# Kernel optimization log

Measured on AMD Instinct MI355X. Metric: run time of the kernel, lower is better.

## Reference

```python
import jax, jax.numpy as jnp
import numpy as np
from jax import lax

B, L = 2, 2048          # batch, seq_len
V = 256                 # vocab
DM = 256                # d_model
DI = 512                # d_inner = 2*d_model (expand=2)
N = 16                  # d_state
R = 16                  # dt_rank = ceil(d_model/16)
K = 4                   # d_conv
NL = 4                  # n_layer
DO = 10                 # d_output
EPS = 1e-5


def setup_inputs() -> dict:
    key = jax.random.key(0)
    ks = jax.random.split(key, 12)
    f = lambda k, shp, s=0.02: (jax.random.normal(k, shp, jnp.float32) * s)
    A_init = jnp.log(jnp.tile(jnp.arange(1, N + 1, dtype=jnp.float32)[None, None, :], (NL, DI, 1)))
    return {
        "input_ids": jax.random.randint(ks[0], (B, L), 0, V, dtype=jnp.int32),
        "emb": f(ks[1], (V, DM)),
        "norm_w": jnp.ones((NL, DM), jnp.float32),
        "norm_b": jnp.zeros((NL, DM), jnp.float32),
        "in_proj_w": f(ks[2], (NL, 2 * DI, DM)),
        "conv_w": f(ks[3], (NL, DI, K), 0.1),
        "conv_b": jnp.zeros((NL, DI), jnp.float32),
        "x_proj_w": f(ks[4], (NL, R + 2 * N, DI)),
        "dt_proj_w": f(ks[5], (NL, DI, R), 0.1),
        "dt_proj_b": f(ks[6], (NL, DI), 0.1),
        "A_log": A_init,
        "Dp": jnp.ones((NL, DI), jnp.float32),
        "out_proj_w": f(ks[7], (NL, DM, DI)),
        "normf_w": jnp.ones((DM,), jnp.float32),
        "normf_b": jnp.zeros((DM,), jnp.float32),
        "dec_w": f(ks[8], (DO, DM)),
        "dec_b": jnp.zeros((DO,), jnp.float32),
    }


def _layer_norm(x, w, b):
    m = x.mean(-1, keepdims=True)
    v = jnp.mean((x - m) ** 2, axis=-1, keepdims=True)
    return (x - m) * lax.rsqrt(v + EPS) * w + b


def _causal_dwconv(x, w, b):
    # x: [B,L,DI], w: [DI,K] depthwise causal conv
    xt = x.transpose(0, 2, 1)  # [B,DI,L]
    out = lax.conv_general_dilated(xt, w[:, None, :], (1,), [(K - 1, 0)],
                                   feature_group_count=DI)
    return (out + b[None, :, None]).transpose(0, 2, 1)


def _selective_scan(deltaA, deltaBu, C):
    # deltaA, deltaBu: [B,L,DI,N]; C: [B,L,N]
    def step(h, inp):
        dA, dBu, c = inp
        h = dA * h + dBu                       # [B,DI,N]
        y = jnp.einsum('bdn,bn->bd', h, c)
        return h, y
    h0 = jnp.zeros(deltaA.shape[:1] + deltaA.shape[2:], deltaA.dtype)
    _, ys = lax.scan(step, h0, (deltaA.transpose(1, 0, 2, 3),
                                deltaBu.transpose(1, 0, 2, 3),
                                C.transpose(1, 0, 2)))
    return ys.transpose(1, 0, 2)  # [B,L,DI]


def _mixer(x, in_w, cw, cb, xp_w, dt_w, dt_b, A_log, Dp, out_w):
    xz = jnp.einsum('bld,ed->ble', x, in_w)        # [B,L,2*DI]
    xm, z = jnp.split(xz, 2, axis=-1)
    xc = jax.nn.silu(_causal_dwconv(xm, cw, cb))   # [B,L,DI]
    x_dbl = jnp.einsum('bld,ed->ble', xc, xp_w)    # [B,L,R+2N]
    dt, Bm, Cm = jnp.split(x_dbl, [R, R + N], axis=-1)
    delta = jax.nn.softplus(jnp.einsum('blr,dr->bld', dt, dt_w) + dt_b)  # [B,L,DI]
    A = -jnp.exp(A_log)                            # [DI,N]
    deltaA = jnp.exp(delta[..., None] * A)         # [B,L,DI,N]
    deltaBu = delta[..., None] * Bm[:, :, None, :] * xc[..., None]
    y = _selective_scan(deltaA, deltaBu, Cm)       # [B,L,DI]
    y = y + Dp * xc
    y = y * jax.nn.silu(z)
    return jnp.einsum('bld,ed->ble', y, out_w)     # [B,L,DM]


def reference(input_ids, emb, norm_w, norm_b, in_proj_w, conv_w, conv_b,
              x_proj_w, dt_proj_w, dt_proj_b, A_log, Dp, out_proj_w,
              normf_w, normf_b, dec_w, dec_b):
    hidden = emb[input_ids]                        # [B,L,DM]
    residual = None
    for i in range(NL):
        residual = hidden + residual if residual is not None else hidden
        h = _layer_norm(residual, norm_w[i], norm_b[i])
        hidden = _mixer(h, in_proj_w[i], conv_w[i], conv_b[i], x_proj_w[i],
                        dt_proj_w[i], dt_proj_b[i], A_log[i], Dp[i], out_proj_w[i])
    residual = hidden + residual
    hidden = _layer_norm(residual, normf_w, normf_b)
    pooled = hidden.mean(axis=1)                   # [B,DM]
    return pooled @ dec_w.T + dec_b                # [B,DO]
```

## Files before the change

### kernel.cpp

```cpp
#include <hip/hip_runtime.h>
#include <hip/hip_bf16.h>

#define BB 2
#define LL 2048
#define DM 256
#define DI 512
#define NST 16
#define RDT 16
#define KC 4
#define NLAY 4
#define DOUT 10
#define XDIM 48
#define TOK (BB*LL)
#define EPSF 1e-5f
#define CHUNK 16
#define NCH (LL/CHUNK)

typedef __bf16 bf16x8 __attribute__((ext_vector_type(8)));
typedef __bf16 bf16x4 __attribute__((ext_vector_type(4)));
typedef float  f32x4  __attribute__((ext_vector_type(4)));

__device__ __forceinline__ float sigmoid_f(float x) { return 1.0f / (1.0f + __expf(-x)); }

__global__ void cast_w_kernel(const float* __restrict__ a, const float* __restrict__ b,
                              const float* __restrict__ c,
                              __bf16* __restrict__ ab, __bf16* __restrict__ bb,
                              __bf16* __restrict__ cbf,
                              int na, int nb, int nc) {
  int stride = gridDim.x * 256;
  for (int i = blockIdx.x*256 + threadIdx.x; i < na; i += stride) ab[i] = (__bf16)a[i];
  for (int i = blockIdx.x*256 + threadIdx.x; i < nb; i += stride) bb[i] = (__bf16)b[i];
  for (int i = blockIdx.x*256 + threadIdx.x; i < nc; i += stride) cbf[i] = (__bf16)c[i];
}

__global__ void add_ln_kernel(float* __restrict__ residual, const float* __restrict__ hidden,
                              const int* __restrict__ ids, const float* __restrict__ emb,
                              const float* __restrict__ w, const float* __restrict__ bia,
                              float* __restrict__ out, __bf16* __restrict__ out_bf,
                              int first, int write32) {
  int t = blockIdx.x, d = threadIdx.x;
  __shared__ float ws8[8];
  float r;
  if (first) r = emb[ids[t]*DM + d];
  else       r = hidden[t*DM + d] + residual[t*DM + d];
  residual[t*DM + d] = r;
  float s = r;
  #pragma unroll
  for (int o = 32; o; o >>= 1) s += __shfl_down(s, o);
  if ((d & 63) == 0) ws8[d >> 6] = s;
  __syncthreads();
  float mean = (ws8[0] + ws8[1] + ws8[2] + ws8[3]) * (1.0f/DM);
  float diff = r - mean;
  float q = diff * diff;
  #pragma unroll
  for (int o = 32; o; o >>= 1) q += __shfl_down(q, o);
  if ((d & 63) == 0) ws8[4 + (d >> 6)] = q;
  __syncthreads();
  float var = (ws8[4] + ws8[5] + ws8[6] + ws8[7]) * (1.0f/DM);
  float v = diff * rsqrtf(var + EPSF) * w[d] + bia[d];
  if (write32) out[t*DM + d] = v;
  out_bf[t*DM + d] = (__bf16)v;
}

__global__ __launch_bounds__(256, 2) void gemm_in_bf16(const __bf16* __restrict__ A,
                                                       const __bf16* __restrict__ W,
                                                       __bf16* __restrict__ xm,
                                                       __bf16* __restrict__ zg) {
  __shared__ __bf16 As[4*64*8];
  __shared__ __bf16 Ws[8*64*8];
  const int K = DM;
  int tid = threadIdx.x;
  int lane = tid & 63, wv = tid >> 6;
  int bm = blockIdx.y * 64, be = blockIdx.x * 128;
  int ss = tid >> 6, sq = (tid >> 4) & 3, sm = tid & 15;
  f32x4 acc[8];
  #pragma unroll
  for (int et = 0; et < 8; ++et) acc[et] = (f32x4){0.f, 0.f, 0.f, 0.f};
  for (int k0 = 0; k0 < K; k0 += 32) {
    bf16x8 av = *(const bf16x8*)&A[(size_t)(bm + ss*16 + sm)*K + k0 + sq*8];
    bf16x8 w0 = *(const bf16x8*)&W[(size_t)(be + ss*16 + sm)*K + k0 + sq*8];
    bf16x8 w1 = *(const bf16x8*)&W[(size_t)(be + 64 + ss*16 + sm)*K + k0 + sq*8];
    __syncthreads();
    *(bf16x8*)&As[((ss*4 + sq)*16 + sm)*8] = av;
    *(bf16x8*)&Ws[((ss*4 + sq)*16 + sm)*8] = w0;
    *(bf16x8*)&Ws[(((4 + ss)*4 + sq)*16 + sm)*8] = w1;
    __syncthreads();
    bf16x8 af = *(const bf16x8*)&As[(wv*64 + lane)*8];
    #pragma unroll
    for (int et = 0; et < 8; ++et) {
      bf16x8 bfr = *(const bf16x8*)&Ws[(et*64 + lane)*8];
      acc[et] = __builtin_amdgcn_mfma_f32_16x16x32_bf16(af, bfr, acc[et], 0, 0, 0);
    }
  }
  int row0 = bm + wv*16 + (lane >> 4)*4;
  int colb = lane & 15;
  #pragma unroll
  for (int et = 0; et < 8; ++et) {
    int col = be + et*16 + colb;
    if (col < DI) {
      #pragma unroll
      for (int r = 0; r < 4; ++r)
        xm[(size_t)(row0 + r)*DI + col] = (__bf16)acc[et][r];
    } else {
      #pragma unroll
      for (int r = 0; r < 4; ++r) {
        float zv = acc[et][r];
        zg[(size_t)(row0 + r)*DI + col - DI] = (__bf16)(zv * sigmoid_f(zv));
      }
    }
  }
}

__global__ __launch_bounds__(256, 2) void gemm_out_bf16(const __bf16* __restrict__ A,
                                                        const __bf16* __restrict__ W,
                                                        float* __restrict__ C) {
  __shared__ __bf16 As[4*64*8];
  __shared__ __bf16 Ws[4*64*8];
  const int K = DI, E = DM;
  int tid = threadIdx.x;
  int lane = tid & 63, wv = tid >> 6;
  int bm = blockIdx.y * 64, be = blockIdx.x * 64;
  int ss = tid >> 6, sq = (tid >> 4) & 3, sm = tid & 15;
  f32x4 acc[4];
  #pragma unroll
  for (int et = 0; et < 4; ++et) acc[et] = (f32x4){0.f, 0.f, 0.f, 0.f};
  for (int k0 = 0; k0 < K; k0 += 32) {
    bf16x8 av = *(const bf16x8*)&A[(size_t)(bm + ss*16 + sm)*K + k0 + sq*8];
    bf16x8 wvv = *(const bf16x8*)&W[(size_t)(be + ss*16 + sm)*K + k0 + sq*8];
    __syncthreads();
    *(bf16x8*)&As[((ss*4 + sq)*16 + sm)*8] = av;
    *(bf16x8*)&Ws[((ss*4 + sq)*16 + sm)*8] = wvv;
    __syncthreads();
    bf16x8 af = *(const bf16x8*)&As[(wv*64 + lane)*8];
    #pragma unroll
    for (int et = 0; et < 4; ++et) {
      bf16x8 bfr = *(const bf16x8*)&Ws[(et*64 + lane)*8];
      acc[et] = __builtin_amdgcn_mfma_f32_16x16x32_bf16(af, bfr, acc[et], 0, 0, 0);
    }
  }
  int row0 = bm + wv*16 + (lane >> 4)*4;
  int col0 = be + (lane & 15);
  #pragma unroll
  for (int et = 0; et < 4; ++et)
    #pragma unroll
    for (int r = 0; r < 4; ++r)
      C[(size_t)(row0 + r)*E + col0 + et*16] = acc[et][r];
}

__global__ __launch_bounds__(512) void xproj_scan1(
    const __bf16* __restrict__ xm, const float* __restrict__ cw,
    const float* __restrict__ cb, const __bf16* __restrict__ Wbf,
    const float* __restrict__ dtw, const float* __restrict__ dtb,
    const float* __restrict__ A_log, const float* __restrict__ Dp,
    float* __restrict__ xdbl, float* __restrict__ hloc,
    float* __restrict__ dsum, float* __restrict__ ylocal,
    float* __restrict__ csout) {
  __shared__ float red[8][3][16][16];
  __shared__ __bf16 xc_s[CHUNK][DI];
  __shared__ __align__(16) float DBC[CHUNK][48];
  int tid = threadIdx.x;
  int lane = tid & 63, w = tid >> 6;
  int bc = blockIdx.x;
  int t0 = bc * CHUNK;
  int b = bc >> 7, c = bc & (NCH - 1);
  int r16 = lane & 15;
  int row = t0 + r16;
  int l = row & (LL - 1);
  int kg = (lane >> 4) * 8;

  f32x4 acc[3];
  #pragma unroll
  for (int e = 0; e < 3; ++e) acc[e] = (f32x4){0.f, 0.f, 0.f, 0.f};
  #pragma unroll
  for (int ks = 0; ks < 2; ++ks) {
    int ch = w*64 + ks*32 + kg;
    bf16x8 v0 = *(const bf16x8*)&xm[(size_t)row*DI + ch];
    bf16x8 v1 = (l >= 1) ? *(const bf16x8*)&xm[(size_t)(row-1)*DI + ch] : (bf16x8)(__bf16)0;
    bf16x8 v2 = (l >= 2) ? *(const bf16x8*)&xm[(size_t)(row-2)*DI + ch] : (bf16x8)(__bf16)0;
    bf16x8 v3 = (l >= 3) ? *(const bf16x8*)&xm[(size_t)(row-3)*DI + ch] : (bf16x8)(__bf16)0;
    bf16x8 a8;
    #pragma unroll
    for (int j = 0; j < 8; ++j) {
      float4 cwv = *(const float4*)&cw[(ch + j)*KC];
      float cv = cb[ch + j];
      cv = fmaf(cwv.x, (float)v3[j], cv);
      cv = fmaf(cwv.y, (float)v2[j], cv);
      cv = fmaf(cwv.z, (float)v1[j], cv);
      cv = fmaf(cwv.w, (float)v0[j], cv);
      a8[j] = (__bf16)(cv * sigmoid_f(cv));
    }
    *(bf16x8*)&xc_s[r16][ch ^ ((r16 & 7) << 3)] = a8;
    #pragma unroll
    for (int e = 0; e < 3; ++e) {
      bf16x8 bv = *(const bf16x8*)&Wbf[(size_t)(e*16 + r16)*DI + ch];
      acc[e] = __builtin_amdgcn_mfma_f32_16x16x32_bf16(a8, bv, acc[e], 0, 0, 0);
    }
  }
  #pragma unroll
  for (int e = 0; e < 3; ++e)
    #pragma unroll
    for (int r = 0; r < 4; ++r)
      red[w][e][(lane >> 4)*4 + r][r16] = acc[e][r];
  __syncthreads();
  for (int idx = tid; idx < 768; idx += 512) {
    int e = idx >> 8, rr = (idx >> 4) & 15, cc = idx & 15;
    float s = 0.f;
    #pragma unroll
    for (int w8 = 0; w8 < 8; ++w8) s += red[w8][e][rr][cc];
    DBC[rr][e*16 + cc] = s;
    xdbl[(size_t)(t0 + rr)*XDIM + e*16 + cc] = s;
  }
  __syncthreads();

  int d = tid;
  float4 wq[4];
  #pragma unroll
  for (int i = 0; i < 4; ++i) wq[i] = *(const float4*)&dtw[(size_t)d*RDT + i*4];
  float dtbv = dtb[d];
  float Dpv = Dp[d];
  float A[NST];
  #pragma unroll
  for (int n = 0; n < NST; ++n) A[n] = -__expf(A_log[d*NST + n]);
  float A0 = A[0];
  bool geo = true;
  #pragma unroll
  for (int n = 1; n < NST; ++n) {
    float ideal = A0 * (float)(n+1);
    geo = geo && (fabsf(A[n] - ideal) <= 1e-5f * fabsf(ideal));
  }
  float h[NST];
  #pragma unroll
  for (int n = 0; n < NST; ++n) h[n] = 0.f;
  float ds = 0.f;
  for (int lp = 0; lp < CHUNK; ++lp) {
    int t = t0 + lp;
    float xcv = (float)xc_s[lp][d ^ ((lp & 7) << 3)];
    float acs = dtbv;
    #pragma unroll
    for (int i = 0; i < 4; ++i) {
      float4 a = *(const float4*)&DBC[lp][i*4];
      acs = fmaf(a.x, wq[i].x, acs); acs = fmaf(a.y, wq[i].y, acs);
      acs = fmaf(a.z, wq[i].z, acs); acs = fmaf(a.w, wq[i].w, acs);
    }
    float del = fmaxf(acs, 0.f) + log1pf(__expf(-fabsf(acs)));
    ds += del;
    float dx = del * xcv;
    float yv = 0.f;
    if (geo) {
      float e = __expf(del * A0);
      float dA = e;
      h[0] = fmaf(dA, h[0], dx * DBC[lp][16]);
      yv = fmaf(h[0], DBC[lp][32], yv);
      #pragma unroll
      for (int n = 1; n < NST; ++n) {
        dA *= e;
        h[n] = fmaf(dA, h[n], dx * DBC[lp][16 + n]);
        yv = fmaf(h[n], DBC[lp][32 + n], yv);
      }
    } else {
      #pragma unroll
      for (int n = 0; n < NST; ++n) {
        h[n] = fmaf(__expf(del * A[n]), h[n], dx * DBC[lp][16 + n]);
        yv = fmaf(h[n], DBC[lp][32 + n], yv);
      }
    }
    yv = fmaf(Dpv, xcv, yv);
    ylocal[(size_t)t*DI + d] = yv;
    csout[(size_t)t*DI + d] = ds;
  }
  #pragma unroll
  for (int n = 0; n < NST; ++n)
    hloc[((size_t)(b*NST + n)*NCH + c)*DI + d] = h[n];
  dsum[(size_t)bc*DI + d] = ds;
}

__global__ __launch_bounds__(64) void scan_pass2(
    const float* __restrict__ hloc, const float* __restrict__ dsum,
    const float* __restrict__ A_log, float* __restrict__ hinit) {
  int g = blockIdx.x*64 + threadIdx.x;
  int d = g & (DI-1);
  int n = (g >> 9) & (NST-1);
  int b = g >> 13;
  float A = -__expf(A_log[d*NST + n]);
  float hc = 0.f;
  size_t base = (size_t)(b*NST + n)*NCH*DI + d;
  #pragma unroll 4
  for (int c = 0; c < NCH; ++c) {
    hinit[base + (size_t)c*DI] = hc;
    float P = __expf(A * dsum[(size_t)(b*NCH + c)*DI + d]);
    hc = fmaf(P, hc, hloc[base + (size_t)c*DI]);
  }
}

__global__ __launch_bounds__(256) void scan_pass3(
    const float* __restrict__ cs, const float* __restrict__ ylocal,
    const __bf16* __restrict__ zg, const float* __restrict__ xdbl,
    const float* __restrict__ A_log, const float* __restrict__ hinit,
    __bf16* __restrict__ y) {
  __shared__ __align__(16) float Cs[CHUNK][16];
  int bc = blockIdx.x >> 1;
  int d  = ((blockIdx.x & 1) << 8) + threadIdx.x;
  int b = bc >> 7, c = bc & (NCH-1);
  int t0 = b*LL + c*CHUNK;
  int tid = threadIdx.x;
  if (tid < CHUNK*4) {
    int row = tid >> 2, q = tid & 3;
    *(float4*)&Cs[row][q*4] = *(const float4*)&xdbl[(size_t)(t0+row)*XDIM + 32 + q*4];
  }
  __syncthreads();
  float A[NST];
  #pragma unroll
  for (int n = 0; n < NST; ++n) A[n] = -__expf(A_log[d*NST + n]);
  float A0 = A[0];
  bool geo = true;
  #pragma unroll
  for (int n = 1; n < NST; ++n) {
    float ideal = A0 * (float)(n+1);
    geo = geo && (fabsf(A[n] - ideal) <= 1e-5f * fabsf(ideal));
  }
  float hin[NST];
  #pragma unroll
  for (int n = 0; n < NST; ++n) hin[n] = hinit[((size_t)(b*NST + n)*NCH + c)*DI + d];
  for (int l = 0; l < CHUNK; ++l) {
    int t = t0 + l;
    float csv = cs[(size_t)t*DI + d];
    float ylv = ylocal[(size_t)t*DI + d];
    float zvg = (float)zg[(size_t)t*DI + d];
    float corr = 0.f;
    if (geo) {
      float g = __expf(csv * A0);
      float dA = g;
      corr = hin[0] * dA * Cs[l][0];
      #pragma unroll
      for (int n = 1; n < NST; ++n) {
        dA *= g;
        corr = fmaf(hin[n] * dA, Cs[l][n], corr);
      }
    } else {
      #pragma unroll
      for (int n = 0; n < NST; ++n)
        corr = fmaf(hin[n] * __expf(A[n] * csv), Cs[l][n], corr);
    }
    y[(size_t)t*DI + d] = (__bf16)((ylv + corr) * zvg);
  }
}

__global__ void pool1_kernel(const float* __restrict__ ln, float* __restrict__ part) {
  int blk = blockIdx.x;
  int b = blk >> 7, c = blk & 127;
  int d = threadIdx.x;
  const float* base = ln + (size_t)b*LL*DM + (size_t)c*16*DM + d;
  float s = 0.f;
  #pragma unroll
  for (int l = 0; l < 16; ++l) s += base[(size_t)l*DM];
  part[(size_t)blk*DM + d] = s;
}

__global__ void pool_decode_kernel(const float* __restrict__ part, const float* __restrict__ dw,
                                   const float* __restrict__ db, float* __restrict__ out) {
  int b = blockIdx.x, d = threadIdx.x;
  __shared__ float pooled[DM];
  float s = 0.f;
  for (int c = 0; c < 128; ++c) s += part[(size_t)(b*128 + c)*DM + d];
  pooled[d] = s * (1.0f/LL);
  __syncthreads();
  if (d < DOUT) {
    float acc = db[d];
    for (int m = 0; m < DM; ++m) acc = fmaf(pooled[m], dw[d*DM + m], acc);
    out[b*DOUT + d] = acc;
  }
}

extern "C" void kernel_launch(void* const* d_in, const int* in_sizes, int n_in,
                              void* d_out, int out_size, void* d_ws, size_t ws_size,
                              hipStream_t stream) {
  const int*   ids     = (const int*)d_in[0];
  const float* emb     = (const float*)d_in[1];
  const float* norm_w  = (const float*)d_in[2];
  const float* norm_b  = (const float*)d_in[3];
  const float* in_w    = (const float*)d_in[4];
  const float* conv_w  = (const float*)d_in[5];
  const float* conv_b  = (const float*)d_in[6];
  const float* xp_w    = (const float*)d_in[7];
  const float* dt_w    = (const float*)d_in[8];
  const float* dt_b    = (const float*)d_in[9];
  const float* A_log   = (const float*)d_in[10];
  const float* Dp      = (const float*)d_in[11];
  const float* out_w   = (const float*)d_in[12];
  const float* normf_w = (const float*)d_in[13];
  const float* normf_b = (const float*)d_in[14];
  const float* dec_w   = (const float*)d_in[15];
  const float* dec_b   = (const float*)d_in[16];
  float* out = (float*)d_out;

  float* ws = (float*)d_ws;
  float* hidden   = ws; ws += TOK*DM;
  float* residual = ws; ws += TOK*DM;
  float* hbuf     = ws; ws += TOK*DM;
  float* xdblbuf  = ws; ws += TOK*XDIM;
  float* hlocbuf  = ws; ws += (size_t)BB*NCH*NST*DI;
  float* hinitbuf = ws; ws += (size_t)BB*NCH*NST*DI;
  float* dsumbuf  = ws; ws += (size_t)BB*NCH*DI;
  float* partbuf  = ws; ws += (size_t)BB*128*DM;
  float* csbuf    = ws; ws += (size_t)TOK*DI;
  float* ylbuf    = ws; ws += (size_t)TOK*DI;
  __bf16* xmbuf   = (__bf16*)ws; ws += TOK*DI/2;
  __bf16* zgbuf   = (__bf16*)ws; ws += TOK*DI/2;
  __bf16* hbuf_bf = (__bf16*)ws; ws += TOK*DM/2;
  __bf16* ybuf_bf = (__bf16*)ws; ws += TOK*DI/2;
  __bf16* inw_bf  = (__bf16*)ws; ws += (size_t)NLAY*2*DI*DM/2;
  __bf16* outw_bf = (__bf16*)ws; ws += (size_t)NLAY*DM*DI/2;
  __bf16* xpw_bf  = (__bf16*)ws; ws += (size_t)NLAY*XDIM*DI/2 + 256;

  const int n_inw = NLAY*2*DI*DM, n_outw = NLAY*DM*DI, n_xpw = NLAY*XDIM*DI;
  cast_w_kernel<<<2048, 256, 0, stream>>>(in_w, out_w, xp_w, inw_bf, outw_bf, xpw_bf,
                                          n_inw, n_outw, n_xpw);

  for (int i = 0; i < NLAY; ++i) {
    add_ln_kernel<<<TOK, DM, 0, stream>>>(residual, hidden, ids, emb,
                                          norm_w + i*DM, norm_b + i*DM,
                                          hbuf, hbuf_bf, i == 0, 0);
    gemm_in_bf16<<<dim3((2*DI)/128, TOK/64), 256, 0, stream>>>(
        hbuf_bf, inw_bf + (size_t)i*2*DI*DM, xmbuf, zgbuf);
    xproj_scan1<<<TOK/CHUNK, 512, 0, stream>>>(
        xmbuf, conv_w + i*DI*KC, conv_b + i*DI,
        xpw_bf + (size_t)i*XDIM*DI,
        dt_w + (size_t)i*DI*RDT, dt_b + i*DI, A_log + (size_t)i*DI*NST,
        Dp + i*DI, xdblbuf, hlocbuf, dsumbuf, ylbuf, csbuf);
    scan_pass2<<<(BB*NST*DI)/64, 64, 0, stream>>>(
        hlocbuf, dsumbuf, A_log + (size_t)i*DI*NST, hinitbuf);
    scan_pass3<<<BB*NCH*(DI/256), 256, 0, stream>>>(
        csbuf, ylbuf, zgbuf, xdblbuf, A_log + (size_t)i*DI*NST,
        hinitbuf, ybuf_bf);
    gemm_out_bf16<<<dim3(DM/64, TOK/64), 256, 0, stream>>>(
        ybuf_bf, outw_bf + (size_t)i*DM*DI, hidden);
  }

  add_ln_kernel<<<TOK, DM, 0, stream>>>(residual, hidden, ids, emb,
                                        normf_w, normf_b, hbuf, hbuf_bf, 0, 1);
  pool1_kernel<<<BB*128, DM, 0, stream>>>(hbuf, partbuf);
  pool_decode_kernel<<<BB, DM, 0, stream>>>(partbuf, dec_w, dec_b, out);
}
```

Baseline: 417.4 us.

## Parallelize chunk-state carry scan across lanes and use one wave per token in layernorm

The inter-chunk carry pass now splits each (b,n,d) chain of 128 chunks across 8 lanes. Each lane computes a 16-chunk segment's decay product and local state, combines the segment prefixes with shuffles, then replays its segment to write initial states. This replaces a 128-step serial dependency per thread, with few threads in flight, by more parallel work. The add+layernorm kernel is rewritten to process one token per wavefront with float4 loads and xor-shuffle reductions, removing shared memory and block syncs. The cost is redundant reads of dsum/hloc in the replay and higher register use for the cached decay factors.

```diff
diff --git a/kernel.cpp b/kernel.cpp
--- a/kernel.cpp
+++ b/kernel.cpp
@@ -38,28 +38,40 @@
                               const float* __restrict__ w, const float* __restrict__ bia,
                               float* __restrict__ out, __bf16* __restrict__ out_bf,
                               int first, int write32) {
-  int t = blockIdx.x, d = threadIdx.x;
-  __shared__ float ws8[8];
-  float r;
-  if (first) r = emb[ids[t]*DM + d];
-  else       r = hidden[t*DM + d] + residual[t*DM + d];
-  residual[t*DM + d] = r;
-  float s = r;
-  #pragma unroll
-  for (int o = 32; o; o >>= 1) s += __shfl_down(s, o);
-  if ((d & 63) == 0) ws8[d >> 6] = s;
-  __syncthreads();
-  float mean = (ws8[0] + ws8[1] + ws8[2] + ws8[3]) * (1.0f/DM);
-  float diff = r - mean;
-  float q = diff * diff;
-  #pragma unroll
-  for (int o = 32; o; o >>= 1) q += __shfl_down(q, o);
-  if ((d & 63) == 0) ws8[4 + (d >> 6)] = q;
-  __syncthreads();
-  float var = (ws8[4] + ws8[5] + ws8[6] + ws8[7]) * (1.0f/DM);
-  float v = diff * rsqrtf(var + EPSF) * w[d] + bia[d];
-  if (write32) out[t*DM + d] = v;
-  out_bf[t*DM + d] = (__bf16)v;
+  int wv = threadIdx.x >> 6, lane = threadIdx.x & 63;
+  int t = blockIdx.x*4 + wv;
+  float4 rv;
+  if (first) {
+    rv = *(const float4*)&emb[(size_t)ids[t]*DM + lane*4];
+  } else {
+    float4 h4 = *(const float4*)&hidden[(size_t)t*DM + lane*4];
+    float4 o4 = *(const float4*)&residual[(size_t)t*DM + lane*4];
+    rv.x = h4.x + o4.x; rv.y = h4.y + o4.y;
+    rv.z = h4.z + o4.z; rv.w = h4.w + o4.w;
+  }
+  *(float4*)&residual[(size_t)t*DM + lane*4] = rv;
+  float s = rv.x + rv.y + rv.z + rv.w;
+  #pragma unroll
+  for (int o = 32; o; o >>= 1) s += __shfl_xor(s, o);
+  float mean = s * (1.0f/DM);
+  float d0 = rv.x - mean, d1 = rv.y - mean, d2 = rv.z - mean, d3 = rv.w - mean;
+  float q = d0*d0 + d1*d1 + d2*d2 + d3*d3;
+  #pragma unroll
+  for (int o = 32; o; o >>= 1) q += __shfl_xor(q, o);
+  float rsig = rsqrtf(q * (1.0f/DM) + EPSF);
+  float4 w4 = *(const float4*)&w[lane*4];
+  float4 b4 = *(const float4*)&bia[lane*4];
+  float v0 = d0*rsig*w4.x + b4.x;
+  float v1 = d1*rsig*w4.y + b4.y;
+  float v2 = d2*rsig*w4.z + b4.z;
+  float v3 = d3*rsig*w4.w + b4.w;
+  if (write32) {
+    float4 o4; o4.x = v0; o4.y = v1; o4.z = v2; o4.w = v3;
+    *(float4*)&out[(size_t)t*DM + lane*4] = o4;
+  }
+  bf16x4 bv;
+  bv[0] = (__bf16)v0; bv[1] = (__bf16)v1; bv[2] = (__bf16)v2; bv[3] = (__bf16)v3;
+  *(bf16x4*)&out_bf[(size_t)t*DM + lane*4] = bv;
 }
 
 __global__ __launch_bounds__(256, 2) void gemm_in_bf16(const __bf16* __restrict__ A,
@@ -274,21 +286,45 @@
   dsum[(size_t)bc*DI + d] = ds;
 }
 
-__global__ __launch_bounds__(64) void scan_pass2(
+__global__ __launch_bounds__(256) void scan_pass2(
     const float* __restrict__ hloc, const float* __restrict__ dsum,
     const float* __restrict__ A_log, float* __restrict__ hinit) {
-  int g = blockIdx.x*64 + threadIdx.x;
-  int d = g & (DI-1);
-  int n = (g >> 9) & (NST-1);
-  int b = g >> 13;
+  int g = blockIdx.x*256 + threadIdx.x;
+  int q = g & 7;
+  int chain = g >> 3;
+  int d = chain & (DI-1);
+  int n = (chain >> 9) & (NST-1);
+  int b = chain >> 13;
   float A = -__expf(A_log[d*NST + n]);
-  float hc = 0.f;
-  size_t base = (size_t)(b*NST + n)*NCH*DI + d;
-  #pragma unroll 4
-  for (int c = 0; c < NCH; ++c) {
-    hinit[base + (size_t)c*DI] = hc;
-    float P = __expf(A * dsum[(size_t)(b*NCH + c)*DI + d]);
-    hc = fmaf(P, hc, hloc[base + (size_t)c*DI]);
+  size_t base  = (size_t)(b*NST + n)*NCH*DI + d;
+  size_t dbase = (size_t)(b*NCH)*DI + d;
+  int c0 = q*16;
+  float Pc[16];
+  float hc = 0.f, Pp = 1.f;
+  #pragma unroll
+  for (int i = 0; i < 16; ++i) {
+    int cc = c0 + i;
+    float P = __expf(A * dsum[dbase + (size_t)cc*DI]);
+    Pc[i] = P;
+    hc = fmaf(P, hc, hloc[base + (size_t)cc*DI]);
+    Pp *= P;
+  }
+  float Pseg = Pp, Bseg = hc;
+  int lane = threadIdx.x & 63;
+  int lb = lane & ~7;
+  float hin = 0.f;
+  #pragma unroll
+  for (int j = 0; j < 7; ++j) {
+    float Pj = __shfl(Pseg, lb + j);
+    float Bj = __shfl(Bseg, lb + j);
+    if (j < q) hin = fmaf(Pj, hin, Bj);
+  }
+  hc = hin;
+  #pragma unroll
+  for (int i = 0; i < 16; ++i) {
+    int cc = c0 + i;
+    hinit[base + (size_t)cc*DI] = hc;
+    hc = fmaf(Pc[i], hc, hloc[base + (size_t)cc*DI]);
   }
 }
 
@@ -417,9 +453,9 @@
                                           n_inw, n_outw, n_xpw);
 
   for (int i = 0; i < NLAY; ++i) {
-    add_ln_kernel<<<TOK, DM, 0, stream>>>(residual, hidden, ids, emb,
-                                          norm_w + i*DM, norm_b + i*DM,
-                                          hbuf, hbuf_bf, i == 0, 0);
+    add_ln_kernel<<<TOK/4, 256, 0, stream>>>(residual, hidden, ids, emb,
+                                             norm_w + i*DM, norm_b + i*DM,
+                                             hbuf, hbuf_bf, i == 0, 0);
     gemm_in_bf16<<<dim3((2*DI)/128, TOK/64), 256, 0, stream>>>(
         hbuf_bf, inw_bf + (size_t)i*2*DI*DM, xmbuf, zgbuf);
     xproj_scan1<<<TOK/CHUNK, 512, 0, stream>>>(
@@ -427,7 +463,7 @@
         xpw_bf + (size_t)i*XDIM*DI,
         dt_w + (size_t)i*DI*RDT, dt_b + i*DI, A_log + (size_t)i*DI*NST,
         Dp + i*DI, xdblbuf, hlocbuf, dsumbuf, ylbuf, csbuf);
-    scan_pass2<<<(BB*NST*DI)/64, 64, 0, stream>>>(
+    scan_pass2<<<(BB*NST*DI*8)/256, 256, 0, stream>>>(
         hlocbuf, dsumbuf, A_log + (size_t)i*DI*NST, hinitbuf);
     scan_pass3<<<BB*NCH*(DI/256), 256, 0, stream>>>(
         csbuf, ylbuf, zgbuf, xdblbuf, A_log + (size_t)i*DI*NST,
@@ -436,8 +472,8 @@
         ybuf_bf, outw_bf + (size_t)i*DM*DI, hidden);
   }
 
-  add_ln_kernel<<<TOK, DM, 0, stream>>>(residual, hidden, ids, emb,
-                                        normf_w, normf_b, hbuf, hbuf_bf, 0, 1);
+  add_ln_kernel<<<TOK/4, 256, 0, stream>>>(residual, hidden, ids, emb,
+                                           normf_w, normf_b, hbuf, hbuf_bf, 0, 1);
   pool1_kernel<<<BB*128, DM, 0, stream>>>(hbuf, partbuf);
   pool_decode_kernel<<<BB, DM, 0, stream>>>(partbuf, dec_w, dec_b, out);
 }
```

Result: faster. 370.4 us (-11.3%).
